# Kernel tuning notes

Measured on AMD Instinct MI355X. Metric: run time of the kernel, lower is better.

## Reference

```python
import jax, jax.numpy as jnp
import numpy as np

L, B, E, H, HID = 2048, 4, 512, 8, 2048
HD = E // H


def setup_inputs() -> dict:
    key = jax.random.key(0)
    ks = jax.random.split(key, 6)
    s = 0.02
    x = jax.random.normal(ks[0], (L, B, E), jnp.float32)
    in_proj_w = jax.random.normal(ks[1], (3 * E, E), jnp.float32) * s
    in_proj_b = jnp.zeros((3 * E,), jnp.float32)
    out_w = jax.random.normal(ks[2], (E, E), jnp.float32) * s
    out_b = jnp.zeros((E,), jnp.float32)
    w1 = jax.random.normal(ks[3], (HID, E), jnp.float32) * s  # torch Linear: (out, in)
    b1 = jnp.zeros((HID,), jnp.float32)
    w2 = jax.random.normal(ks[4], (E, HID), jnp.float32) * s
    b2 = jnp.zeros((E,), jnp.float32)
    ln_g = jnp.ones((E,), jnp.float32)
    ln_b = jnp.zeros((E,), jnp.float32)
    return {"x": x, "in_proj_w": in_proj_w, "in_proj_b": in_proj_b,
            "out_w": out_w, "out_b": out_b, "w1": w1, "b1": b1,
            "w2": w2, "b2": b2, "ln_g": ln_g, "ln_b": ln_b}


def _pos_encoding(S, Emb, dtype):
    # even i: sin((t+1) * 10000^(-i/E)); odd i: cos((t+1) * 10000^(-(i+1)/E))
    t = jnp.arange(S, dtype=dtype)[:, None]
    i = jnp.arange(Emb, dtype=dtype)[None, :]
    even = jnp.sin((t + 1.0) * jnp.power(10000.0, -i / Emb))
    odd = jnp.cos((t + 1.0) * jnp.power(10000.0, -(i + 1.0) / Emb))
    return jnp.where(jnp.arange(Emb)[None, :] % 2 == 0, even, odd)  # (S, Emb)


def _layernorm(x, g, b, eps=1e-5):
    mu = jnp.mean(x, axis=-1, keepdims=True)
    var = jnp.mean(jnp.square(x - mu), axis=-1, keepdims=True)
    return (x - mu) * jax.lax.rsqrt(var + eps) * g + b


def _mha(x, in_proj_w, in_proj_b, out_w, out_b):
    # x: (L, B, E); self-attention, torch MultiheadAttention semantics
    qkv = jnp.einsum('lbe,fe->lbf', x, in_proj_w) + in_proj_b
    q, k, v = jnp.split(qkv, 3, axis=-1)
    q = q.reshape(L, B, H, HD)
    k = k.reshape(L, B, H, HD)
    v = v.reshape(L, B, H, HD)
    scores = jnp.einsum('lbhd,mbhd->bhlm', q, k) / np.sqrt(HD).astype(np.float32)
    attn = jax.nn.softmax(scores, axis=-1)
    o = jnp.einsum('bhlm,mbhd->lbhd', attn, v).reshape(L, B, E)
    return jnp.einsum('lbe,fe->lbf', o, out_w) + out_b


def reference(x, in_proj_w, in_proj_b, out_w, out_b, w1, b1, w2, b2, ln_g, ln_b):
    # positional encoding: varies along dim1, broadcasts along dim0 (as in source)
    pe = _pos_encoding(x.shape[1], x.shape[2], x.dtype)  # (B, E)
    x = x + pe[None, :, :]
    # Post-Norm path
    x = _layernorm(_mha(x, in_proj_w, in_proj_b, out_w, out_b) + x, ln_g, ln_b)
    h = jax.nn.gelu(jnp.einsum('lbe,he->lbh', x, w1) + b1, approximate=False)
    ff = jnp.einsum('lbh,eh->lbe', h, w2) + b2
    x = _layernorm(ff + x, ln_g, ln_b)
    return x
```

## Files before the change

kernel.cpp:

```cpp
#include <hip/hip_runtime.h>

typedef unsigned short u16;
typedef unsigned int   u32;
typedef u16  u16x2 __attribute__((ext_vector_type(2)));
typedef u16  u16x4 __attribute__((ext_vector_type(4)));
typedef u16  u16x8 __attribute__((ext_vector_type(8)));
typedef short s8v  __attribute__((ext_vector_type(8)));
typedef float f4v  __attribute__((ext_vector_type(4)));
typedef u32  u32x2 __attribute__((ext_vector_type(2)));
typedef u32  u32x4 __attribute__((ext_vector_type(4)));

#define L_SEQ 2048
#define B_SZ  4
#define E_DIM 512
#define H_CNT 8
#define HD    64
#define HID   2048
#define M_ROWS (L_SEQ * B_SZ)
#define QSCALE 0.18033688011112042f

__device__ __forceinline__ u16 f2b(float f) {
    unsigned u = __builtin_bit_cast(unsigned, f);
    u += 0x7fffu + ((u >> 16) & 1u);
    return (u16)(u >> 16);
}
__device__ __forceinline__ float b2f(u16 u) {
    u32 x = ((u32)u) << 16; return __builtin_bit_cast(float, x);
}
#if defined(__has_builtin)
#if __has_builtin(__builtin_amdgcn_cvt_pk_bf16_f32)
#define HAVE_PK_BF16 1
#endif
#if __has_builtin(__builtin_amdgcn_rcpf)
#define HAVE_RCPF 1
#endif
#endif
__device__ __forceinline__ u32 pk_trunc(float a, float b) {
#ifdef HAVE_PK_BF16
    typedef __bf16 bf2 __attribute__((ext_vector_type(2)));
    bf2 r = __builtin_amdgcn_cvt_pk_bf16_f32(a, b);
    return __builtin_bit_cast(u32, r);
#else
    u32 ua = __builtin_bit_cast(u32, a), ub = __builtin_bit_cast(u32, b);
    return (ua >> 16) | (ub & 0xffff0000u);
#endif
}
__device__ __forceinline__ float frcp(float x) {
#ifdef HAVE_RCPF
    return __builtin_amdgcn_rcpf(x);
#else
    return 1.0f / x;
#endif
}
__device__ __forceinline__ void gload_lds16(const u16* g, u16* l) {
    __builtin_amdgcn_global_load_lds((__attribute__((address_space(1))) void*)(u16*)g,
                                     (__attribute__((address_space(3))) void*)l, 16, 0, 0);
}
__device__ __forceinline__ float gelu_f(float v) {
    float y2 = v * (1.5957691216f + 0.0713548576f * v * v);
    return v / (1.0f + __expf(-y2));
}

__global__ __launch_bounds__(256) void pe_tab_k(float* __restrict__ pet) {
    int i = blockIdx.x * 256 + threadIdx.x;
    int e = i & (E_DIM - 1);
    float t = (float)(i >> 9) + 1.0f;
    int ee = (e & 1) ? (e + 1) : e;
    float w = exp2f((-(float)ee / 512.0f) * 13.287712379549449f);
    pet[i] = (e & 1) ? cosf(t * w) : sinf(t * w);
}

__global__ __launch_bounds__(256) void pe_add_k(const float* __restrict__ x,
                                                const float* __restrict__ pet,
                                                u16* __restrict__ xpb) {
    int idx = (blockIdx.x * 256 + threadIdx.x) * 4;
    f4v v = *(const f4v*)(x + idx);
    f4v p = *(const f4v*)(pet + (idx & 2047));
    u16x4 o;
#pragma unroll
    for (int i = 0; i < 4; ++i) o[i] = f2b(v[i] + p[i]);
    *(u16x4*)(xpb + idx) = o;
}

__global__ __launch_bounds__(256) void conv4_k(const float* __restrict__ s1, u16* __restrict__ d1, int n1,
                                               const float* __restrict__ s2, u16* __restrict__ d2, int n2,
                                               const float* __restrict__ s3, u16* __restrict__ d3, int n3,
                                               const float* __restrict__ s4, u16* __restrict__ d4) {
    int o = (blockIdx.x * 256 + threadIdx.x) * 4;
    const float* s; u16* d;
    if (o < n1) { s = s1; d = d1; }
    else { o -= n1;
        if (o < n2) { s = s2; d = d2; }
        else { o -= n2;
            if (o < n3) { s = s3; d = d3; }
            else { o -= n3; s = s4; d = d4; } } }
    f4v v = *(const f4v*)(s + o);
    u16x4 q;
#pragma unroll
    for (int i = 0; i < 4; ++i) q[i] = f2b(v[i]);
    *(u16x4*)(d + o) = q;
}

template <int NP, bool WRITEF, bool WRITEB>
__global__ __launch_bounds__(256)
void ln_c(const u16* __restrict__ p0, const u16* __restrict__ p1,
          const u16* __restrict__ p2, const u16* __restrict__ p3,
          const float* __restrict__ bias, const u16* __restrict__ resid,
          const float* __restrict__ gw, const float* __restrict__ bw,
          float* __restrict__ outF, u16* __restrict__ outB) {
    int wave = threadIdx.x >> 6, lane = threadIdx.x & 63;
    size_t row = (size_t)blockIdx.x * 4 + wave;
    size_t off = row * E_DIM + lane * 8;
    u16x8 rv = *(const u16x8*)(resid + off);
    f4v a, b;
#pragma unroll
    for (int i = 0; i < 4; ++i) { a[i] = b2f(rv[i]); b[i] = b2f(rv[i + 4]); }
    a += *(const f4v*)(bias + lane * 8);
    b += *(const f4v*)(bias + lane * 8 + 4);
    const u16* ps[4] = {p0, p1, p2, p3};
#pragma unroll
    for (int z = 0; z < NP; ++z) {
        u16x8 t = *(const u16x8*)(ps[z] + off);
#pragma unroll
        for (int i = 0; i < 4; ++i) { a[i] += b2f(t[i]); b[i] += b2f(t[i + 4]); }
    }
    float s = (a[0] + a[1]) + (a[2] + a[3]) + (b[0] + b[1]) + (b[2] + b[3]);
#pragma unroll
    for (int o = 1; o < 64; o <<= 1) s += __shfl_xor(s, o, 64);
    float mu = s * (1.0f / E_DIM);
    float q = 0.f;
#pragma unroll
    for (int i = 0; i < 4; ++i) { float d = a[i] - mu; q += d * d; }
#pragma unroll
    for (int i = 0; i < 4; ++i) { float d = b[i] - mu; q += d * d; }
#pragma unroll
    for (int o = 1; o < 64; o <<= 1) q += __shfl_xor(q, o, 64);
    float rstd = rsqrtf(q * (1.0f / E_DIM) + 1e-5f);
    f4v g0 = *(const f4v*)(gw + lane * 8), g1 = *(const f4v*)(gw + lane * 8 + 4);
    f4v w0 = *(const f4v*)(bw + lane * 8), w1 = *(const f4v*)(bw + lane * 8 + 4);
    f4v y0, y1;
#pragma unroll
    for (int i = 0; i < 4; ++i) { y0[i] = (a[i] - mu) * rstd * g0[i] + w0[i];
                                  y1[i] = (b[i] - mu) * rstd * g1[i] + w1[i]; }
    if (WRITEF) {
        *(f4v*)(outF + off)     = y0;
        *(f4v*)(outF + off + 4) = y1;
    }
    if (WRITEB) {
        u16x8 o;
#pragma unroll
        for (int i = 0; i < 4; ++i) { o[i] = f2b(y0[i]); o[i + 4] = f2b(y1[i]); }
        *(u16x8*)(outB + off) = o;
    }
}

__global__ __launch_bounds__(256) void transpose_v_k(const u16* __restrict__ vb,
                                                     u16* __restrict__ vt) {
    __shared__ __align__(16) u16 T[64 * 66];
    int t = threadIdx.x;
    int lt = blockIdx.x, bh = blockIdx.y;
    const u16* src = vb + (size_t)bh * (L_SEQ * HD) + (size_t)lt * 64 * HD;
    int lr = t >> 2, d0 = (t & 3) * 16;
    s8v va = *(const s8v*)(src + lr * HD + d0);
    s8v vb8 = *(const s8v*)(src + lr * HD + d0 + 8);
#pragma unroll
    for (int c = 0; c < 4; ++c) {
        u16x2 p0; p0[0] = (u16)va[c * 2]; p0[1] = (u16)va[c * 2 + 1];
        u16x2 p1; p1[0] = (u16)vb8[c * 2]; p1[1] = (u16)vb8[c * 2 + 1];
        *(u16x2*)(&T[lr * 66 + d0 + c * 2])     = p0;
        *(u16x2*)(&T[lr * 66 + d0 + 8 + c * 2]) = p1;
    }
    __syncthreads();
    int d = t >> 2, l0 = (t & 3) * 16;
    u16 tmp[16];
#pragma unroll
    for (int i = 0; i < 16; ++i) tmp[i] = T[(l0 + i) * 66 + d];
    u16* dst = vt + (size_t)bh * (L_SEQ * HD) + (size_t)d * L_SEQ + lt * 64 + l0;
    u16x8 o0, o1;
#pragma unroll
    for (int i = 0; i < 8; ++i) { o0[i] = tmp[i]; o1[i] = tmp[8 + i]; }
    *(u16x8*)dst       = o0;
    *(u16x8*)(dst + 8) = o1;
}

__global__ __launch_bounds__(256, 4)
void gemm_ks(const u16* __restrict__ A, const u16* __restrict__ Bw,
             int N, int K, int Kper,
             u16* __restrict__ q0, u16* __restrict__ q1) {
    __shared__ __align__(16) u16 As[2][128 * 32];
    __shared__ __align__(16) u16 Bs[2][128 * 32];
    const int tid = threadIdx.x;
    const int wave = tid >> 6, lane = tid & 63;
    const int col = lane & 15, quad = lane >> 4;
    const int n = blockIdx.x;
    const int xcd = n & 7, loc = n >> 3;
    const int bn = (loc & 3) * 128;
    const int bm = (xcd * 8 + ((loc >> 2) & 7)) * 128;
    const int kz = loc >> 5;
    u16* pz = kz ? q1 : q0;
    const int wm = (wave >> 1) * 64, wn = (wave & 1) * 64;
    f4v acc[4][4] = {};
    const int srow = wave * 16 + (lane >> 2);
    const int soff = (lane & 3) * 8;
    const u16* Ag = A + (size_t)(bm + srow) * K + kz * Kper + soff;
    const u16* Bg = Bw + (size_t)(bn + srow) * K + kz * Kper + soff;
    const int wo = wave * 512;
    gload_lds16(Ag,                  &As[0][wo]);
    gload_lds16(Ag + (size_t)64 * K, &As[0][wo + 2048]);
    gload_lds16(Bg,                  &Bs[0][wo]);
    gload_lds16(Bg + (size_t)64 * K, &Bs[0][wo + 2048]);
    const int nit = Kper >> 5;
    for (int t = 0; t < nit; ++t) {
        const int cur = t & 1, nxt = cur ^ 1;
        __syncthreads();
        if (t + 1 < nit) {
            const int kc = (t + 1) * 32;
            gload_lds16(Ag + kc,                  &As[nxt][wo]);
            gload_lds16(Ag + (size_t)64 * K + kc, &As[nxt][wo + 2048]);
            gload_lds16(Bg + kc,                  &Bs[nxt][wo]);
            gload_lds16(Bg + (size_t)64 * K + kc, &Bs[nxt][wo + 2048]);
        }
        s8v af[4], bf[4];
#pragma unroll
        for (int i = 0; i < 4; ++i) af[i] = *(const s8v*)(&As[cur][(wm + i * 16 + col) * 32 + quad * 8]);
#pragma unroll
        for (int j = 0; j < 4; ++j) bf[j] = *(const s8v*)(&Bs[cur][(wn + j * 16 + col) * 32 + quad * 8]);
#pragma unroll
        for (int i = 0; i < 4; ++i)
#pragma unroll
            for (int j = 0; j < 4; ++j)
                acc[i][j] = __builtin_amdgcn_mfma_f32_16x16x32_bf16(af[i], bf[j], acc[i][j], 0, 0, 0);
    }
#pragma unroll
    for (int j = 0; j < 4; ++j) {
        int gn = bn + wn + j * 16 + col;
#pragma unroll
        for (int i = 0; i < 4; ++i) {
            int m0 = bm + wm + i * 16 + quad * 4;
#pragma unroll
            for (int r = 0; r < 4; ++r)
                pz[(size_t)(m0 + r) * N + gn] = f2b(acc[i][j][r]);
        }
    }
}

#define G28_STAGE(Ad, Bd, kf)                                                          \
    {                                                                                  \
        _Pragma("unroll")                                                              \
        for (int s = 0; s < 2; ++s) {                                                  \
            const int qa = s * 512 + tid;                                              \
            const int rhoA = qa >> 2;                                                  \
            gload_lds16(A + (size_t)(bm + rhoA) * Ka + koff + (kf) + gsw, (Ad) + qa * 8); \
        }                                                                              \
        {                                                                              \
            const int rhoB = tid >> 2;                                                 \
            gload_lds16(Bw + (size_t)(bn + rhoB) * Kb + koff + (kf) + gsw, (Bd) + tid * 8); \
        }                                                                              \
    }

#define G28_COMPUTE(Ab_, Bb_)                                                          \
    {                                                                                  \
        s8v bfr[4], afr[4];                                                            \
        _Pragma("unroll")                                                              \
        for (int j = 0; j < 4; ++j) {                                                  \
            const int rB = wc * 64 + j * 16 + col;                                     \
            bfr[j] = *(const s8v*)((Bb_) + rB * 32 + ((quad ^ ((rB >> 1) & 3)) * 8));  \
        }                                                                              \
        _Pragma("unroll")                                                              \
        for (int i = 0; i < 4; ++i) {                                                  \
            const int rA = wr * 64 + i * 16 + col;                                     \
            afr[i] = *(const s8v*)((Ab_) + rA * 32 + ((quad ^ ((rA >> 1) & 3)) * 8));  \
        }                                                                              \
        __builtin_amdgcn_s_setprio(1);                                                 \
        _Pragma("unroll")                                                              \
        for (int i = 0; i < 4; ++i)                                                    \
            _Pragma("unroll")                                                          \
            for (int j = 0; j < 4; ++j)                                                \
                acc[i][j] = __builtin_amdgcn_mfma_f32_16x16x32_bf16(afr[i], bfr[j], acc[i][j], 0, 0, 0); \
        __builtin_amdgcn_s_setprio(0);                                                 \
    }

template <int MODE, int NTL, int KZL, int KTILES>
__global__ __launch_bounds__(512, 2)
void g28(const u16* __restrict__ A, const u16* __restrict__ Bw,
         const float* __restrict__ bias, int Ka, int Kb, int N,
         u16* __restrict__ o0, u16* __restrict__ o1, u16* __restrict__ o2) {
    extern __shared__ __align__(16) u16 LDS[];
    const int tid = threadIdx.x;
    const int wave = tid >> 6, lane = tid & 63;
    const int col = lane & 15, quad = lane >> 4;
    const int wr = wave >> 1, wc = wave & 1;
    const int n = blockIdx.x;
    const int xcd = n & 7, loc = n >> 3;
    const int mt = xcd * 4 + (loc & 3);
    const int rest = loc >> 2;
    const int nt = (NTL == 1) ? 0 : (rest % NTL);
    const int kz = (KZL == 1) ? 0 : (rest / NTL);
    const int bm = mt * 256, bn = nt * 128;
    const int koff = kz * (KTILES * 32);
    const int gsw = ((lane & 3) ^ ((lane >> 3) & 3)) * 8;
    f4v acc[4][4] = {};
    u16* A0 = LDS;          u16* B0 = LDS + 8192;
    u16* A1 = LDS + 12288;  u16* B1 = LDS + 20480;
    u16* A2 = LDS + 24576;  u16* B2 = LDS + 32768;
    G28_STAGE(A0, B0, 0);
    G28_STAGE(A1, B1, 32);
    asm volatile("s_waitcnt vmcnt(3)" ::: "memory");
    __builtin_amdgcn_s_barrier();
    __builtin_amdgcn_sched_barrier(0);
    for (int t = 0; t < KTILES - 2; ++t) {
        G28_STAGE(A2, B2, (t + 2) * 32);
        G28_COMPUTE(A0, B0);
        asm volatile("s_waitcnt vmcnt(3)" ::: "memory");
        __builtin_amdgcn_s_barrier();
        __builtin_amdgcn_sched_barrier(0);
        u16* ta = A0; A0 = A1; A1 = A2; A2 = ta;
        u16* tb = B0; B0 = B1; B1 = B2; B2 = tb;
    }
    G28_COMPUTE(A0, B0);
    asm volatile("s_waitcnt vmcnt(0)" ::: "memory");
    __builtin_amdgcn_s_barrier();
    __builtin_amdgcn_sched_barrier(0);
    G28_COMPUTE(A1, B1);
#pragma unroll
    for (int j = 0; j < 4; ++j) {
        const int gn = bn + wc * 64 + j * 16 + col;
        if (MODE == 0) {
            const float bv = bias[gn];
            const int which = gn >> 9, hh = (gn >> 6) & 7, d = gn & 63;
            u16* dst = (which == 0) ? o0 : (which == 1) ? o1 : o2;
            const float qs = (which == 0) ? QSCALE : 1.0f;
#pragma unroll
            for (int i = 0; i < 4; ++i) {
                const int m0 = bm + wr * 64 + i * 16 + quad * 4;
#pragma unroll
                for (int r = 0; r < 4; ++r) {
                    const int m = m0 + r;
                    const int l = m >> 2, bb = m & 3;
                    dst[((size_t)(bb * H_CNT + hh) * L_SEQ + l) * HD + d] = f2b((acc[i][j][r] + bv) * qs);
                }
            }
        } else if (MODE == 2) {
            const float bv = bias[gn];
#pragma unroll
            for (int i = 0; i < 4; ++i) {
                const int m0 = bm + wr * 64 + i * 16 + quad * 4;
#pragma unroll
                for (int r = 0; r < 4; ++r)
                    o0[(size_t)(m0 + r) * N + gn] = f2b(gelu_f(acc[i][j][r] + bv));
            }
        } else {
            u16* pz = (kz == 0) ? o0 : o1;
#pragma unroll
            for (int i = 0; i < 4; ++i) {
                const int m0 = bm + wr * 64 + i * 16 + quad * 4;
#pragma unroll
                for (int r = 0; r < 4; ++r)
                    pz[(size_t)(m0 + r) * N + gn] = f2b(acc[i][j][r]);
            }
        }
    }
}

__global__ __launch_bounds__(512, 4)
void attn_k(const u16* __restrict__ qg, const u16* __restrict__ kg,
            const u16* __restrict__ vtg, u16* __restrict__ og) {
    __shared__ __align__(16) u16 KV[2][2][2][2][64 * 32];
    __shared__ float LSB[2][256];
    const int tid = threadIdx.x;
    const int wave = tid >> 6, lane = tid & 63;
    const int grp = wave >> 2, w4 = wave & 3;
    const int col = lane & 15, quad = lane >> 4;
    const int flat = blockIdx.x;
    const int xcd = flat & 7, loc = flat >> 3;
    const int bh = xcd * 4 + (loc >> 4);
    const int qc = loc & 15;
    const size_t base = (size_t)bh * (L_SEQ * HD);
    s8v qf[2][2];
#pragma unroll
    for (int t = 0; t < 2; ++t) {
        const int qrow = qc * 128 + w4 * 32 + t * 16 + col;
#pragma unroll
        for (int hh = 0; hh < 2; ++hh)
            qf[t][hh] = *(const s8v*)(qg + base + (size_t)qrow * HD + hh * 32 + quad * 8);
    }
    f4v oa[2][4] = {};
    float ls0 = 0.f, ls1 = 0.f;
    const int h = w4 & 1, r0 = (w4 >> 1) * 16;
    const int srow = lane >> 2, c = lane & 3;
    const int cp = c ^ ((srow >> 1) & 3);
    const int sig = ((srow >> 2) << 3) + ((r0 >> 4) << 2) + (srow & 3);
    const u16* Kg = kg + base + (size_t)(sig + grp * 1024) * HD + h * 32 + cp * 8;
    const u16* Vg = vtg + base + (size_t)(r0 + srow) * L_SEQ + grp * 1024 + h * 32 + cp * 8;
    {
        gload_lds16(Kg,                      &KV[grp][0][0][h][r0 * 32]);
        gload_lds16(Kg + (size_t)32 * HD,    &KV[grp][0][0][h][(r0 + 32) * 32]);
        gload_lds16(Vg,                      &KV[grp][1][0][h][r0 * 32]);
        gload_lds16(Vg + (size_t)32 * L_SEQ, &KV[grp][1][0][h][(r0 + 32) * 32]);
    }
    const int perm = (col >> 1) & 3;
    for (int it = 0; it < 16; ++it) {
        const int cur = it & 1, nxt = cur ^ 1;
        __syncthreads();
        if (it + 1 < 16) {
            const int kv0 = (it + 1) * 64;
            gload_lds16(Kg + (size_t)kv0 * HD,         &KV[grp][0][nxt][h][r0 * 32]);
            gload_lds16(Kg + (size_t)(kv0 + 32) * HD,  &KV[grp][0][nxt][h][(r0 + 32) * 32]);
            gload_lds16(Vg + kv0,                      &KV[grp][1][nxt][h][r0 * 32]);
            gload_lds16(Vg + kv0 + (size_t)32 * L_SEQ, &KV[grp][1][nxt][h][(r0 + 32) * 32]);
        }
        f4v st[2][4];
#pragma unroll
        for (int j = 0; j < 4; ++j) {
            s8v k0 = *(const s8v*)(&KV[grp][0][cur][0][(j * 16 + col) * 32 + ((quad ^ perm) * 8)]);
            s8v k1 = *(const s8v*)(&KV[grp][0][cur][1][(j * 16 + col) * 32 + ((quad ^ perm) * 8)]);
#pragma unroll
            for (int t = 0; t < 2; ++t) {
                f4v z = {};
                z = __builtin_amdgcn_mfma_f32_16x16x32_bf16(k0, qf[t][0], z, 0, 0, 0);
                z = __builtin_amdgcn_mfma_f32_16x16x32_bf16(k1, qf[t][1], z, 0, 0, 0);
                st[t][j] = z;
            }
        }
        u32 pk[2][4][2];
#pragma unroll
        for (int t = 0; t < 2; ++t)
#pragma unroll
            for (int j = 0; j < 4; ++j) {
                f4v p;
#pragma unroll
                for (int r = 0; r < 4; ++r) p[r] = __builtin_amdgcn_exp2f(st[t][j][r]);
                float psum = (p[0] + p[1]) + (p[2] + p[3]);
                if (t == 0) ls0 += psum; else ls1 += psum;
                pk[t][j][0] = pk_trunc(p[0], p[1]);
                pk[t][j][1] = pk_trunc(p[2], p[3]);
            }
#pragma unroll
        for (int c2 = 0; c2 < 2; ++c2) {
            s8v pf[2];
#pragma unroll
            for (int t = 0; t < 2; ++t) {
                u32x4 q4 = {pk[t][2 * c2][0], pk[t][2 * c2][1],
                            pk[t][2 * c2 + 1][0], pk[t][2 * c2 + 1][1]};
                pf[t] = __builtin_bit_cast(s8v, q4);
            }
#pragma unroll
            for (int dj = 0; dj < 4; ++dj) {
                s8v vf = *(const s8v*)(&KV[grp][1][cur][c2][(dj * 16 + col) * 32 + ((quad ^ perm) * 8)]);
#pragma unroll
                for (int t = 0; t < 2; ++t)
                    oa[t][dj] = __builtin_amdgcn_mfma_f32_16x16x32_bf16(pf[t], vf, oa[t][dj], 0, 0, 0);
            }
        }
    }
    ls0 += __shfl_xor(ls0, 16, 64); ls0 += __shfl_xor(ls0, 32, 64);
    ls1 += __shfl_xor(ls1, 16, 64); ls1 += __shfl_xor(ls1, 32, 64);
    float* cmb = (float*)&KV[1][0][0][0][0];
    const int slot = w4 * 64 + lane;
    if (grp == 1) {
#pragma unroll
        for (int t = 0; t < 2; ++t)
#pragma unroll
            for (int dj = 0; dj < 4; ++dj)
                *(f4v*)(cmb + ((size_t)(t * 4 + dj) * 256 + slot) * 4) = oa[t][dj];
        LSB[0][slot] = ls0;
        LSB[1][slot] = ls1;
    }
    __syncthreads();
    if (grp == 0) {
#pragma unroll
        for (int t = 0; t < 2; ++t)
#pragma unroll
            for (int dj = 0; dj < 4; ++dj)
                oa[t][dj] += *(const f4v*)(cmb + ((size_t)(t * 4 + dj) * 256 + slot) * 4);
        ls0 += LSB[0][slot];
        ls1 += LSB[1][slot];
        const int b = bh >> 3, hd = bh & 7;
#pragma unroll
        for (int t = 0; t < 2; ++t)
#pragma unroll
            for (int r = 0; r < 4; ++r) {
                float lv = __shfl(t == 0 ? ls0 : ls1, quad * 4 + r, 64);
                float inv = frcp(lv);
                int lrow = qc * 128 + w4 * 32 + t * 16 + quad * 4 + r;
                size_t mrow = (size_t)(lrow * 4 + b) * E_DIM + hd * HD;
#pragma unroll
                for (int dj = 0; dj < 4; ++dj)
                    og[mrow + dj * 16 + col] = f2b(oa[t][dj][r] * inv);
            }
    }
}

extern "C" void kernel_launch(void* const* d_in, const int* in_sizes, int n_in,
                              void* d_out, int out_size, void* d_ws, size_t ws_size,
                              hipStream_t stream) {
    const float* x     = (const float*)d_in[0];
    const float* w_qkv = (const float*)d_in[1];
    const float* b_qkv = (const float*)d_in[2];
    const float* w_out = (const float*)d_in[3];
    const float* b_out = (const float*)d_in[4];
    const float* w1    = (const float*)d_in[5];
    const float* b1    = (const float*)d_in[6];
    const float* w2    = (const float*)d_in[7];
    const float* b2    = (const float*)d_in[8];
    const float* ln_g  = (const float*)d_in[9];
    const float* ln_b  = (const float*)d_in[10];

    char* ws = (char*)d_ws;
    u16*   WQKV = (u16*)(ws + 0);
    u16*   WOUT = (u16*)(ws + 1572864);
    u16*   W1B  = (u16*)(ws + 2097152);
    u16*   W2B  = (u16*)(ws + 4194304);
    u16*   XPB  = (u16*)(ws + 6291456);
    u16*   QB   = (u16*)(ws + 14680064);
    u16*   KB   = (u16*)(ws + 23068672);
    u16*   VB   = (u16*)(ws + 31457280);
    u16*   VT   = (u16*)(ws + 39845888);
    float* PET  = (float*)(ws + 82837504);
    u16*   OB   = VB;
    u16*   OP0  = (u16*)(ws + 48234496);
    u16*   OP1  = (u16*)(ws + 56623104);
    u16*   X3B  = QB;
    u16*   HB   = (u16*)(ws + 48234496);
    u16*   FP0  = XPB;
    u16*   FP1  = KB;

    static bool attr_done = false;
    if (!attr_done) {
        hipFuncSetAttribute((const void*)g28<0, 12, 1, 16>,
                            hipFuncAttributeMaxDynamicSharedMemorySize, 73728);
        hipFuncSetAttribute((const void*)g28<2, 16, 1, 16>,
                            hipFuncAttributeMaxDynamicSharedMemorySize, 73728);
        hipFuncSetAttribute((const void*)g28<3, 4, 2, 32>,
                            hipFuncAttributeMaxDynamicSharedMemorySize, 73728);
        attr_done = true;
    }

    pe_tab_k<<<8, 256, 0, stream>>>(PET);
    pe_add_k<<<4096, 256, 0, stream>>>(x, PET, XPB);
    conv4_k<<<3072, 256, 0, stream>>>(w_qkv, WQKV, 3 * E_DIM * E_DIM,
                                      w_out, WOUT, E_DIM * E_DIM,
                                      w1, W1B, HID * E_DIM,
                                      w2, W2B);
    g28<0, 12, 1, 16><<<384, 512, 73728, stream>>>(XPB, WQKV, b_qkv, E_DIM, E_DIM, 0,
                                                   QB, KB, VB);
    transpose_v_k<<<dim3(32, 32), 256, 0, stream>>>(VB, VT);
    attn_k<<<512, 512, 0, stream>>>(QB, KB, VT, OB);
    gemm_ks<<<512, 256, 0, stream>>>(OB, WOUT, E_DIM, E_DIM, 256, OP0, OP1);
    ln_c<2, false, true><<<2048, 256, 0, stream>>>(OP0, OP1, nullptr, nullptr,
                                                   b_out, XPB, ln_g, ln_b, nullptr, X3B);
    g28<2, 16, 1, 16><<<512, 512, 73728, stream>>>(X3B, W1B, b1, E_DIM, E_DIM, HID,
                                                   HB, nullptr, nullptr);
    g28<3, 4, 2, 32><<<256, 512, 73728, stream>>>(HB, W2B, nullptr, HID, HID, E_DIM,
                                                  FP0, FP1, nullptr);
    ln_c<2, true, false><<<2048, 256, 0, stream>>>(FP0, FP1, nullptr, nullptr,
                                                   b2, X3B, ln_g, ln_b, (float*)d_out, nullptr);
}
```

Baseline: 230.9 us.

## Fuse V transpose into QKV GEMM epilogue and merge prep kernels

The QKV GEMM epilogue now stages the V tile through LDS and writes it directly in transposed (b,h,d,l) layout, which removes the separate transpose_v_k kernel and its extra read/write pass over V. The pe_add and weight-conversion kernels are merged into one launch. This saves two kernel launches and one round trip of V through global memory. The cost is an extra LDS staging pass and more barriers in the GEMM tail for the V-producing blocks.

New measurement: 223.7 us. 1.03x faster.

```diff
diff --git a/kernel.cpp b/kernel.cpp
--- a/kernel.cpp
+++ b/kernel.cpp
@@ -70,35 +70,37 @@
     pet[i] = (e & 1) ? cosf(t * w) : sinf(t * w);
 }
 
-__global__ __launch_bounds__(256) void pe_add_k(const float* __restrict__ x,
-                                                const float* __restrict__ pet,
-                                                u16* __restrict__ xpb) {
-    int idx = (blockIdx.x * 256 + threadIdx.x) * 4;
-    f4v v = *(const f4v*)(x + idx);
-    f4v p = *(const f4v*)(pet + (idx & 2047));
-    u16x4 o;
-#pragma unroll
-    for (int i = 0; i < 4; ++i) o[i] = f2b(v[i] + p[i]);
-    *(u16x4*)(xpb + idx) = o;
-}
-
-__global__ __launch_bounds__(256) void conv4_k(const float* __restrict__ s1, u16* __restrict__ d1, int n1,
-                                               const float* __restrict__ s2, u16* __restrict__ d2, int n2,
-                                               const float* __restrict__ s3, u16* __restrict__ d3, int n3,
-                                               const float* __restrict__ s4, u16* __restrict__ d4) {
-    int o = (blockIdx.x * 256 + threadIdx.x) * 4;
-    const float* s; u16* d;
-    if (o < n1) { s = s1; d = d1; }
-    else { o -= n1;
-        if (o < n2) { s = s2; d = d2; }
-        else { o -= n2;
-            if (o < n3) { s = s3; d = d3; }
-            else { o -= n3; s = s4; d = d4; } } }
-    f4v v = *(const f4v*)(s + o);
-    u16x4 q;
-#pragma unroll
-    for (int i = 0; i < 4; ++i) q[i] = f2b(v[i]);
-    *(u16x4*)(d + o) = q;
+__global__ __launch_bounds__(256) void prep_k(const float* __restrict__ x,
+                                              const float* __restrict__ pet,
+                                              u16* __restrict__ xpb,
+                                              const float* __restrict__ s1, u16* __restrict__ d1, int n1,
+                                              const float* __restrict__ s2, u16* __restrict__ d2, int n2,
+                                              const float* __restrict__ s3, u16* __restrict__ d3, int n3,
+                                              const float* __restrict__ s4, u16* __restrict__ d4) {
+    int bid = blockIdx.x;
+    if (bid < 4096) {
+        int idx = (bid * 256 + threadIdx.x) * 4;
+        f4v v = *(const f4v*)(x + idx);
+        f4v p = *(const f4v*)(pet + (idx & 2047));
+        u16x4 o;
+#pragma unroll
+        for (int i = 0; i < 4; ++i) o[i] = f2b(v[i] + p[i]);
+        *(u16x4*)(xpb + idx) = o;
+    } else {
+        int o = ((bid - 4096) * 256 + threadIdx.x) * 4;
+        const float* s; u16* d;
+        if (o < n1) { s = s1; d = d1; }
+        else { o -= n1;
+            if (o < n2) { s = s2; d = d2; }
+            else { o -= n2;
+                if (o < n3) { s = s3; d = d3; }
+                else { o -= n3; s = s4; d = d4; } } }
+        f4v v = *(const f4v*)(s + o);
+        u16x4 q;
+#pragma unroll
+        for (int i = 0; i < 4; ++i) q[i] = f2b(v[i]);
+        *(u16x4*)(d + o) = q;
+    }
 }
 
 template <int NP, bool WRITEF, bool WRITEB>
@@ -152,35 +154,6 @@
         for (int i = 0; i < 4; ++i) { o[i] = f2b(y0[i]); o[i + 4] = f2b(y1[i]); }
         *(u16x8*)(outB + off) = o;
     }
-}
-
-__global__ __launch_bounds__(256) void transpose_v_k(const u16* __restrict__ vb,
-                                                     u16* __restrict__ vt) {
-    __shared__ __align__(16) u16 T[64 * 66];
-    int t = threadIdx.x;
-    int lt = blockIdx.x, bh = blockIdx.y;
-    const u16* src = vb + (size_t)bh * (L_SEQ * HD) + (size_t)lt * 64 * HD;
-    int lr = t >> 2, d0 = (t & 3) * 16;
-    s8v va = *(const s8v*)(src + lr * HD + d0);
-    s8v vb8 = *(const s8v*)(src + lr * HD + d0 + 8);
-#pragma unroll
-    for (int c = 0; c < 4; ++c) {
-        u16x2 p0; p0[0] = (u16)va[c * 2]; p0[1] = (u16)va[c * 2 + 1];
-        u16x2 p1; p1[0] = (u16)vb8[c * 2]; p1[1] = (u16)vb8[c * 2 + 1];
-        *(u16x2*)(&T[lr * 66 + d0 + c * 2])     = p0;
-        *(u16x2*)(&T[lr * 66 + d0 + 8 + c * 2]) = p1;
-    }
-    __syncthreads();
-    int d = t >> 2, l0 = (t & 3) * 16;
-    u16 tmp[16];
-#pragma unroll
-    for (int i = 0; i < 16; ++i) tmp[i] = T[(l0 + i) * 66 + d];
-    u16* dst = vt + (size_t)bh * (L_SEQ * HD) + (size_t)d * L_SEQ + lt * 64 + l0;
-    u16x8 o0, o1;
-#pragma unroll
-    for (int i = 0; i < 8; ++i) { o0[i] = tmp[i]; o1[i] = tmp[8 + i]; }
-    *(u16x8*)dst       = o0;
-    *(u16x8*)(dst + 8) = o1;
 }
 
 __global__ __launch_bounds__(256, 4)
@@ -322,13 +295,39 @@
     __builtin_amdgcn_s_barrier();
     __builtin_amdgcn_sched_barrier(0);
     G28_COMPUTE(A1, B1);
+    if (MODE == 0 && nt >= 8) {
+        __syncthreads();
+        u16* xb = LDS;
+#pragma unroll
+        for (int j = 0; j < 4; ++j) {
+            const int ln = wc * 64 + j * 16 + col;
+            const float bv = bias[nt * 128 + ln];
+#pragma unroll
+            for (int i = 0; i < 4; ++i) {
+                const int lm = wr * 64 + i * 16 + quad * 4;
+#pragma unroll
+                for (int r = 0; r < 4; ++r)
+                    xb[ln * 264 + lm + r] = f2b(acc[i][j][r] + bv);
+            }
+        }
+        __syncthreads();
+        const int l0 = bm >> 2;
+        for (int rr = 0; rr < 64; ++rr) {
+            const int rid = wave * 64 + rr;
+            const int ln = rid >> 2, b = rid & 3;
+            const int h = (nt - 8) * 2 + (ln >> 6), d = ln & 63;
+            u16 v = xb[ln * 264 + lane * 4 + b];
+            o2[((size_t)(b * H_CNT + h) * HD + d) * L_SEQ + l0 + lane] = v;
+        }
+        return;
+    }
 #pragma unroll
     for (int j = 0; j < 4; ++j) {
         const int gn = bn + wc * 64 + j * 16 + col;
         if (MODE == 0) {
             const float bv = bias[gn];
             const int which = gn >> 9, hh = (gn >> 6) & 7, d = gn & 63;
-            u16* dst = (which == 0) ? o0 : (which == 1) ? o1 : o2;
+            u16* dst = (which == 0) ? o0 : o1;
             const float qs = (which == 0) ? QSCALE : 1.0f;
 #pragma unroll
             for (int i = 0; i < 4; ++i) {
@@ -537,14 +536,13 @@
     }
 
     pe_tab_k<<<8, 256, 0, stream>>>(PET);
-    pe_add_k<<<4096, 256, 0, stream>>>(x, PET, XPB);
-    conv4_k<<<3072, 256, 0, stream>>>(w_qkv, WQKV, 3 * E_DIM * E_DIM,
-                                      w_out, WOUT, E_DIM * E_DIM,
-                                      w1, W1B, HID * E_DIM,
-                                      w2, W2B);
+    prep_k<<<7168, 256, 0, stream>>>(x, PET, XPB,
+                                     w_qkv, WQKV, 3 * E_DIM * E_DIM,
+                                     w_out, WOUT, E_DIM * E_DIM,
+                                     w1, W1B, HID * E_DIM,
+                                     w2, W2B);
     g28<0, 12, 1, 16><<<384, 512, 73728, stream>>>(XPB, WQKV, b_qkv, E_DIM, E_DIM, 0,
-                                                   QB, KB, VB);
-    transpose_v_k<<<dim3(32, 32), 256, 0, stream>>>(VB, VT);
+                                                   QB, KB, VT);
     attn_k<<<512, 512, 0, stream>>>(QB, KB, VT, OB);
     gemm_ks<<<512, 256, 0, stream>>>(OB, WOUT, E_DIM, E_DIM, 256, OP0, OP1);
     ln_c<2, false, true><<<2048, 256, 0, stream>>>(OP0, OP1, nullptr, nullptr,
```
